# Kernel optimization log

Hardware: AMD Instinct MI355X
Metric: run time of the kernel (lower is better)

The kernel has to match this reference:

```python
import jax, jax.numpy as jnp
import numpy as np


def setup_inputs() -> dict:
    key = jax.random.key(0)
    ks = jax.random.split(key, 5)
    B, S, D, H, dk = 4, 2048, 1024, 16, 64
    s = 0.02
    return {
        "x": jax.random.normal(ks[0], (B, S, D), dtype=jnp.float32),
        "Wq": jax.random.normal(ks[1], (H, D, dk), dtype=jnp.float32) * s,
        "Wk": jax.random.normal(ks[2], (H, D, dk), dtype=jnp.float32) * s,
        "Wv": jax.random.normal(ks[3], (H, D, dk), dtype=jnp.float32) * s,
        "Wo": jax.random.normal(ks[4], (H * dk, D), dtype=jnp.float32) * s,
    }


def reference(x, Wq, Wk, Wv, Wo):
    # Per-head projections: [B,S,D] x [H,D,dk] -> [B,H,S,dk]
    Q = jnp.einsum("bsd,hdk->bhsk", x, Wq)
    K = jnp.einsum("bsd,hdk->bhsk", x, Wk)
    V = jnp.einsum("bsd,hdk->bhsk", x, Wv)
    scale = 1.0 / jnp.sqrt(jnp.asarray(Wq.shape[-1], x.dtype))
    scores = jnp.einsum("bhqk,bhsk->bhqs", Q, K) * scale  # [B,H,S,S]
    attn = jax.nn.softmax(scores, axis=-1)
    out = jnp.einsum("bhqs,bhsk->bhqk", attn, V)  # [B,H,S,dk]
    B, H, S, dk = out.shape
    # concat heads along feature dim (matches torch.cat over head outputs)
    out = out.transpose(0, 2, 1, 3).reshape(B, S, H * dk)
    return out @ Wo  # [B,S,D]
```

## Files before the change

kernel.cpp:

```cpp
#include <hip/hip_runtime.h>
#include <hip/hip_bf16.h>
#include <stdint.h>

typedef __attribute__((ext_vector_type(8))) short bf16x8;
typedef __attribute__((ext_vector_type(4))) float f32x4;
typedef __attribute__((ext_vector_type(4))) unsigned short us4;

#define AS1C(p) ((const __attribute__((address_space(1))) void*)(p))
#define AS3(p)  ((__attribute__((address_space(3))) void*)(p))

#if __has_builtin(__builtin_amdgcn_exp2f)
#define EXP2(x) __builtin_amdgcn_exp2f(x)
#else
#define EXP2(x) __expf((x) * 0.69314718f)
#endif

#define MAX3(a,b,c) fmaxf(fmaxf((a),(b)),(c))

static __device__ __forceinline__ unsigned short f2b(float f) {
  union { __hip_bfloat16 h; unsigned short u; } cv;
  cv.h = __float2bfloat16(f);
  return cv.u;
}

static __device__ __forceinline__ unsigned int cvtpk(float a, float b) {
  unsigned int r;
  asm("v_cvt_pk_bf16_f32 %0, %1, %2" : "=v"(r) : "v"(a), "v"(b));
  return r;
}

__global__ __launch_bounds__(256) void conv_x_kernel(const float* __restrict__ x,
                                                     unsigned short* __restrict__ xb,
                                                     int n4) {
  int i = blockIdx.x * 256 + threadIdx.x;
  if (i >= n4) return;
  float4 v = ((const float4*)x)[i];
  us4 r = { f2b(v.x), f2b(v.y), f2b(v.z), f2b(v.w) };
  *(us4*)&xb[(size_t)i * 4] = r;
}

__global__ __launch_bounds__(256) void conv_wqkv_kernel(const float* __restrict__ Wq,
                                                        const float* __restrict__ Wk,
                                                        const float* __restrict__ Wv,
                                                        unsigned short* __restrict__ WqkvT) {
  int bid = blockIdx.x;
  int which = bid >> 8;
  int h  = (bid >> 4) & 15;
  int dt = bid & 15;
  const float* W = (which == 0) ? Wq : (which == 1 ? Wk : Wv);
  __shared__ float tile[64][65];
  const int t = threadIdx.x;
  const int c  = t & 63;
  const int r0 = t >> 6;
  const float* src = W + (size_t)h * 65536 + (size_t)dt * 64 * 64;
#pragma unroll
  for (int it = 0; it < 16; ++it) {
    int r = r0 + it * 4;
    tile[r][c] = src[r * 64 + c];
  }
  __syncthreads();
  const size_t n0 = (size_t)which * 1024 + h * 64;
  const int d0 = dt * 64;
#pragma unroll
  for (int it = 0; it < 16; ++it) {
    int cc = r0 + it * 4;
    WqkvT[(n0 + cc) * 1024 + d0 + c] = f2b(tile[c][cc]);
  }
}

__global__ __launch_bounds__(256) void conv_wo_kernel(const float* __restrict__ Wo,
                                                      unsigned short* __restrict__ WoT) {
  int kt = blockIdx.x >> 4, nt = blockIdx.x & 15;
  __shared__ float tile[64][65];
  const int t = threadIdx.x;
  const int c  = t & 63;
  const int r0 = t >> 6;
  const float* src = Wo + (size_t)(kt * 64) * 1024 + nt * 64;
#pragma unroll
  for (int it = 0; it < 16; ++it) {
    int r = r0 + it * 4;
    tile[r][c] = src[(size_t)r * 1024 + c];
  }
  __syncthreads();
#pragma unroll
  for (int it = 0; it < 16; ++it) {
    int cc = r0 + it * 4;
    WoT[((size_t)nt * 64 + cc) * 1024 + kt * 64 + c] = f2b(tile[c][cc]);
  }
}

__global__ __launch_bounds__(256) void gemm_qkv_kernel(
    const unsigned short* __restrict__ A,
    const unsigned short* __restrict__ Bt,
    unsigned short* __restrict__ Q,
    unsigned short* __restrict__ Ko,
    unsigned short* __restrict__ Vt) {
  __shared__ __align__(16) unsigned short sA[128 * 32];
  __shared__ __align__(16) unsigned short sB[128 * 32];
  const int tid  = threadIdx.x;
  const int lane = tid & 63;
  const int wid  = tid >> 6;
  const int wr = wid >> 1, wc = wid & 1;
  const int brow = blockIdx.y * 128;
  const int bcol = blockIdx.x * 128;
  const int K = 1024;

  f32x4 acc[4][4] = {};

  const int r4 = tid >> 2;
  const int c8 = (tid & 3) * 8;
  const unsigned short* ga = A  + (size_t)(brow + r4) * K + c8;
  const unsigned short* gb = Bt + (size_t)(bcol + r4) * K + c8;
  unsigned short* lAw = sA + wid * 512;
  unsigned short* lBw = sB + wid * 512;

  for (int kb = 0; kb < K; kb += 32) {
    if (kb) __syncthreads();
    __builtin_amdgcn_global_load_lds(AS1C(ga + kb),            AS3(lAw),        16, 0, 0);
    __builtin_amdgcn_global_load_lds(AS1C(ga + 64 * K + kb),   AS3(lAw + 2048), 16, 0, 0);
    __builtin_amdgcn_global_load_lds(AS1C(gb + kb),            AS3(lBw),        16, 0, 0);
    __builtin_amdgcn_global_load_lds(AS1C(gb + 64 * K + kb),   AS3(lBw + 2048), 16, 0, 0);
    __syncthreads();

    bf16x8 af[4], bfr[4];
#pragma unroll
    for (int mi = 0; mi < 4; ++mi)
      af[mi] = *(const bf16x8*)&sA[(wr * 64 + mi * 16 + (lane & 15)) * 32 + (lane >> 4) * 8];
#pragma unroll
    for (int ni = 0; ni < 4; ++ni)
      bfr[ni] = *(const bf16x8*)&sB[(wc * 64 + ni * 16 + (lane & 15)) * 32 + (lane >> 4) * 8];
#pragma unroll
    for (int mi = 0; mi < 4; ++mi)
#pragma unroll
      for (int ni = 0; ni < 4; ++ni)
        acc[mi][ni] = __builtin_amdgcn_mfma_f32_16x16x32_bf16(af[mi], bfr[ni], acc[mi][ni], 0, 0, 0);
  }

#pragma unroll
  for (int mi = 0; mi < 4; ++mi) {
    int row0 = brow + wr * 64 + mi * 16 + (lane >> 4) * 4;
    int b = row0 >> 11, s0 = row0 & 2047;
#pragma unroll
    for (int ni = 0; ni < 4; ++ni) {
      int col = bcol + wc * 64 + ni * 16 + (lane & 15);
      int which = col >> 10;
      int h  = (col >> 6) & 15;
      int kk = col & 63;
      if (which == 2) {
        us4 pk = { f2b(acc[mi][ni][0]), f2b(acc[mi][ni][1]),
                   f2b(acc[mi][ni][2]), f2b(acc[mi][ni][3]) };
        *(us4*)&Vt[((size_t)(b * 16 + h) * 64 + kk) * 2048 + s0] = pk;
      } else {
        unsigned short* dst = (which == 0) ? Q : Ko;
        float scl = (which == 0) ? 0.18033688f : 1.0f;
#pragma unroll
        for (int j = 0; j < 4; ++j)
          dst[((size_t)(b * 16 + h) * 2048 + (s0 + j)) * 64 + kk] = f2b(acc[mi][ni][j] * scl);
      }
    }
  }
}

__global__ __launch_bounds__(256) void gemm_out_kernel(
    const unsigned short* __restrict__ A,
    const unsigned short* __restrict__ Bt,
    float* __restrict__ out) {
  __shared__ __align__(16) unsigned short sA[128 * 32];
  __shared__ __align__(16) unsigned short sB[128 * 32];
  const int tid  = threadIdx.x;
  const int lane = tid & 63;
  const int wid  = tid >> 6;
  const int wr = wid >> 1, wc = wid & 1;
  const int brow = blockIdx.y * 128;
  const int bcol = blockIdx.x * 128;
  const int K = 1024;

  f32x4 acc[4][4] = {};

  const int r4 = tid >> 2;
  const int c8 = (tid & 3) * 8;
  const unsigned short* ga = A  + (size_t)(brow + r4) * K + c8;
  const unsigned short* gb = Bt + (size_t)(bcol + r4) * K + c8;
  unsigned short* lAw = sA + wid * 512;
  unsigned short* lBw = sB + wid * 512;

  for (int kb = 0; kb < K; kb += 32) {
    if (kb) __syncthreads();
    __builtin_amdgcn_global_load_lds(AS1C(ga + kb),          AS3(lAw),        16, 0, 0);
    __builtin_amdgcn_global_load_lds(AS1C(ga + 64 * K + kb), AS3(lAw + 2048), 16, 0, 0);
    __builtin_amdgcn_global_load_lds(AS1C(gb + kb),          AS3(lBw),        16, 0, 0);
    __builtin_amdgcn_global_load_lds(AS1C(gb + 64 * K + kb), AS3(lBw + 2048), 16, 0, 0);
    __syncthreads();

    bf16x8 af[4], bfr[4];
#pragma unroll
    for (int mi = 0; mi < 4; ++mi)
      af[mi] = *(const bf16x8*)&sA[(wr * 64 + mi * 16 + (lane & 15)) * 32 + (lane >> 4) * 8];
#pragma unroll
    for (int ni = 0; ni < 4; ++ni)
      bfr[ni] = *(const bf16x8*)&sB[(wc * 64 + ni * 16 + (lane & 15)) * 32 + (lane >> 4) * 8];
#pragma unroll
    for (int mi = 0; mi < 4; ++mi)
#pragma unroll
      for (int ni = 0; ni < 4; ++ni)
        acc[mi][ni] = __builtin_amdgcn_mfma_f32_16x16x32_bf16(af[mi], bfr[ni], acc[mi][ni], 0, 0, 0);
  }

#pragma unroll
  for (int mi = 0; mi < 4; ++mi) {
    int row0 = brow + wr * 64 + mi * 16 + (lane >> 4) * 4;
#pragma unroll
    for (int ni = 0; ni < 4; ++ni) {
      int col = bcol + wc * 64 + ni * 16 + (lane & 15);
#pragma unroll
      for (int j = 0; j < 4; ++j)
        out[(size_t)(row0 + j) * 1024 + col] = acc[mi][ni][j];
    }
  }
}

__global__ __launch_bounds__(512) void attn_kernel(
    const unsigned short* __restrict__ Q,
    const unsigned short* __restrict__ K,
    const unsigned short* __restrict__ Vt,
    unsigned short* __restrict__ O) {
  __shared__ __align__(16) unsigned short sK[64 * 72];
  __shared__ __align__(16) unsigned short sVt[64 * 72];
  __shared__ __align__(16) unsigned short sP[8][16 * 72];

  const int tid = threadIdx.x, lane = tid & 63, w = tid >> 6;
  const int l15 = lane & 15, hi = lane >> 4;
  const int n = blockIdx.x + (blockIdx.y << 4);
  const int bh = (n & 7) * 8 + ((n >> 3) >> 4);
  const int qx = (n >> 3) & 15;
  const int qb = qx * 128;
  const unsigned short* Qp  = Q  + (size_t)bh * 131072;
  const unsigned short* Kp  = K  + (size_t)bh * 131072;
  const unsigned short* Vtp = Vt + (size_t)bh * 131072;

  const int qrow = qb + w * 16 + l15;
  bf16x8 qf0 = *(const bf16x8*)&Qp[(size_t)qrow * 64 + hi * 8];
  bf16x8 qf1 = *(const bf16x8*)&Qp[(size_t)qrow * 64 + 32 + hi * 8];

  f32x4 o[4] = {};
  float m_ = 0.f;
  float l_ = 0.f;

  const int sr  = tid >> 3;
  const int sc8 = (tid & 7) * 8;
  const unsigned short* kptr = Kp  + (size_t)sr * 64 + sc8;
  const unsigned short* vptr = Vtp + (size_t)sr * 2048 + sc8;

  bf16x8 rk = *(const bf16x8*)kptr;
  bf16x8 rv = *(const bf16x8*)vptr;

  for (int kt = 0; kt < 32; ++kt) {
    __syncthreads();
    *(bf16x8*)&sK[sr * 72 + sc8]  = rk;
    *(bf16x8*)&sVt[sr * 72 + sc8] = rv;
    __syncthreads();

    if (kt < 31) {
      kptr += 4096; vptr += 64;
      rk = *(const bf16x8*)kptr;
      rv = *(const bf16x8*)vptr;
    }

    f32x4 sc[4] = {};
    __builtin_amdgcn_s_setprio(1);
#pragma unroll
    for (int ni = 0; ni < 4; ++ni) {
      bf16x8 kf0 = *(const bf16x8*)&sK[(ni * 16 + l15) * 72 + hi * 8];
      bf16x8 kf1 = *(const bf16x8*)&sK[(ni * 16 + l15) * 72 + 32 + hi * 8];
      sc[ni] = __builtin_amdgcn_mfma_f32_16x16x32_bf16(kf0, qf0, sc[ni], 0, 0, 0);
      sc[ni] = __builtin_amdgcn_mfma_f32_16x16x32_bf16(kf1, qf1, sc[ni], 0, 0, 0);
    }
    __builtin_amdgcn_s_setprio(0);

    float t0 = MAX3(sc[0][0], sc[0][1], sc[0][2]);
    float t1 = MAX3(sc[0][3], sc[1][0], sc[1][1]);
    float t2 = MAX3(sc[1][2], sc[1][3], sc[2][0]);
    float t3 = MAX3(sc[2][1], sc[2][2], sc[2][3]);
    float t4 = MAX3(sc[3][0], sc[3][1], sc[3][2]);
    float pmax = fmaxf(MAX3(t0, t1, t2), MAX3(t3, t4, sc[3][3]));

    if (!__all(pmax - m_ <= 8.0f)) {
      pmax = fmaxf(pmax, __shfl_xor(pmax, 16));
      pmax = fmaxf(pmax, __shfl_xor(pmax, 32));
      float mnew  = fmaxf(m_, pmax);
      float alpha = EXP2(m_ - mnew);
      l_ *= alpha;
#pragma unroll
      for (int j = 0; j < 4; ++j) {
        float aj = __shfl(alpha, hi * 4 + j);
#pragma unroll
        for (int ni = 0; ni < 4; ++ni) o[ni][j] *= aj;
      }
      m_ = mnew;
    }

    const float mcur = m_;
    f32x4 sum4 = {};
#pragma unroll
    for (int ni = 0; ni < 4; ++ni)
#pragma unroll
      for (int r = 0; r < 4; ++r) {
        float p = EXP2(sc[ni][r] - mcur);
        sc[ni][r] = p;
        sum4[r] += p;
      }
    l_ += (sum4[0] + sum4[1]) + (sum4[2] + sum4[3]);

    unsigned short* pb = &sP[w][l15 * 72];
#pragma unroll
    for (int ni = 0; ni < 4; ++ni) {
      uint2 pk = { cvtpk(sc[ni][0], sc[ni][1]), cvtpk(sc[ni][2], sc[ni][3]) };
      *(uint2*)&pb[ni * 16 + hi * 4] = pk;
    }

    bf16x8 pa0 = *(const bf16x8*)&sP[w][l15 * 72 + hi * 8];
    bf16x8 pa1 = *(const bf16x8*)&sP[w][l15 * 72 + 32 + hi * 8];
    __builtin_amdgcn_s_setprio(1);
#pragma unroll
    for (int ni = 0; ni < 4; ++ni) {
      bf16x8 vf0 = *(const bf16x8*)&sVt[(ni * 16 + l15) * 72 + hi * 8];
      bf16x8 vf1 = *(const bf16x8*)&sVt[(ni * 16 + l15) * 72 + 32 + hi * 8];
      o[ni] = __builtin_amdgcn_mfma_f32_16x16x32_bf16(pa0, vf0, o[ni], 0, 0, 0);
      o[ni] = __builtin_amdgcn_mfma_f32_16x16x32_bf16(pa1, vf1, o[ni], 0, 0, 0);
    }
    __builtin_amdgcn_s_setprio(0);
  }

  l_ += __shfl_xor(l_, 16);
  l_ += __shfl_xor(l_, 32);
  float linv = 1.0f / l_;

  const int b = bh >> 4, h = bh & 15;
#pragma unroll
  for (int j = 0; j < 4; ++j) {
    float inv = __shfl(linv, hi * 4 + j);
    int row = qb + w * 16 + hi * 4 + j;
#pragma unroll
    for (int ni = 0; ni < 4; ++ni)
      O[((size_t)b * 2048 + row) * 1024 + h * 64 + ni * 16 + l15] = f2b(o[ni][j] * inv);
  }
}

extern "C" void kernel_launch(void* const* d_in, const int* in_sizes, int n_in,
                              void* d_out, int out_size, void* d_ws, size_t ws_size,
                              hipStream_t stream) {
  const float* x  = (const float*)d_in[0];
  const float* Wq = (const float*)d_in[1];
  const float* Wk = (const float*)d_in[2];
  const float* Wv = (const float*)d_in[3];
  const float* Wo = (const float*)d_in[4];
  float* out = (float*)d_out;

  char* w = (char*)d_ws;
  unsigned short* xb   = (unsigned short*)(w);
  unsigned short* wqkv = (unsigned short*)(w + 16777216);
  unsigned short* wo   = (unsigned short*)(w + 23068672);
  unsigned short* Qb   = (unsigned short*)(w + 25165824);
  unsigned short* Kb   = (unsigned short*)(w + 41943040);
  unsigned short* Vtb  = (unsigned short*)(w + 58720256);
  unsigned short* Ob   = (unsigned short*)(w + 75497472);

  conv_x_kernel<<<8192, 256, 0, stream>>>(x, xb, 2097152);
  conv_wqkv_kernel<<<768, 256, 0, stream>>>(Wq, Wk, Wv, wqkv);
  conv_wo_kernel<<<256, 256, 0, stream>>>(Wo, wo);
  gemm_qkv_kernel<<<dim3(24, 64), 256, 0, stream>>>(xb, wqkv, Qb, Kb, Vtb);
  attn_kernel<<<dim3(16, 64), 512, 0, stream>>>(Qb, Kb, Vtb, Ob);
  gemm_out_kernel<<<dim3(8, 64), 256, 0, stream>>>(Ob, wo, out);
}
```

Measured before the change: 210.8 us.

## Double-buffer K/V tiles via direct global-to-LDS loads with XOR swizzle

Result: faster. 199.7 us (-5.3%).

```diff
diff --git a/kernel.cpp b/kernel.cpp
--- a/kernel.cpp
+++ b/kernel.cpp
@@ -224,8 +224,8 @@
     const unsigned short* __restrict__ K,
     const unsigned short* __restrict__ Vt,
     unsigned short* __restrict__ O) {
-  __shared__ __align__(16) unsigned short sK[64 * 72];
-  __shared__ __align__(16) unsigned short sVt[64 * 72];
+  __shared__ __align__(16) unsigned short sK[2][64 * 64];
+  __shared__ __align__(16) unsigned short sVt[2][64 * 64];
   __shared__ __align__(16) unsigned short sP[8][16 * 72];
 
   const int tid = threadIdx.x, lane = tid & 63, w = tid >> 6;
@@ -246,32 +246,39 @@
   float m_ = 0.f;
   float l_ = 0.f;
 
-  const int sr  = tid >> 3;
-  const int sc8 = (tid & 7) * 8;
-  const unsigned short* kptr = Kp  + (size_t)sr * 64 + sc8;
-  const unsigned short* vptr = Vtp + (size_t)sr * 2048 + sc8;
-
-  bf16x8 rk = *(const bf16x8*)kptr;
-  bf16x8 rv = *(const bf16x8*)vptr;
+  const int lrow = lane >> 3;
+  const int uch  = (lane & 7) ^ lrow;
+  const unsigned short* kg = Kp  + (size_t)(w * 8 + lrow) * 64   + uch * 8;
+  const unsigned short* vg = Vtp + (size_t)(w * 8 + lrow) * 2048 + uch * 8;
+  unsigned short* dK0 = &sK[0][w * 512];
+  unsigned short* dK1 = &sK[1][w * 512];
+  unsigned short* dV0 = &sVt[0][w * 512];
+  unsigned short* dV1 = &sVt[1][w * 512];
+
+  const int x7 = l15 & 7;
+  const int ck0 = (hi ^ x7) * 8;
+  const int ck1 = ((hi + 4) ^ x7) * 8;
+
+  __builtin_amdgcn_global_load_lds(AS1C(kg), AS3(dK0), 16, 0, 0);
+  __builtin_amdgcn_global_load_lds(AS1C(vg), AS3(dV0), 16, 0, 0);
+  __syncthreads();
 
   for (int kt = 0; kt < 32; ++kt) {
-    __syncthreads();
-    *(bf16x8*)&sK[sr * 72 + sc8]  = rk;
-    *(bf16x8*)&sVt[sr * 72 + sc8] = rv;
-    __syncthreads();
-
+    const int cur = kt & 1;
     if (kt < 31) {
-      kptr += 4096; vptr += 64;
-      rk = *(const bf16x8*)kptr;
-      rv = *(const bf16x8*)vptr;
-    }
+      kg += 4096; vg += 64;
+      __builtin_amdgcn_global_load_lds(AS1C(kg), AS3(cur ? dK0 : dK1), 16, 0, 0);
+      __builtin_amdgcn_global_load_lds(AS1C(vg), AS3(cur ? dV0 : dV1), 16, 0, 0);
+    }
+    const unsigned short* sKc  = &sK[cur][0];
+    const unsigned short* sVtc = &sVt[cur][0];
 
     f32x4 sc[4] = {};
     __builtin_amdgcn_s_setprio(1);
 #pragma unroll
     for (int ni = 0; ni < 4; ++ni) {
-      bf16x8 kf0 = *(const bf16x8*)&sK[(ni * 16 + l15) * 72 + hi * 8];
-      bf16x8 kf1 = *(const bf16x8*)&sK[(ni * 16 + l15) * 72 + 32 + hi * 8];
+      bf16x8 kf0 = *(const bf16x8*)&sKc[(ni * 16 + l15) * 64 + ck0];
+      bf16x8 kf1 = *(const bf16x8*)&sKc[(ni * 16 + l15) * 64 + ck1];
       sc[ni] = __builtin_amdgcn_mfma_f32_16x16x32_bf16(kf0, qf0, sc[ni], 0, 0, 0);
       sc[ni] = __builtin_amdgcn_mfma_f32_16x16x32_bf16(kf1, qf1, sc[ni], 0, 0, 0);
     }
@@ -323,12 +330,14 @@
     __builtin_amdgcn_s_setprio(1);
 #pragma unroll
     for (int ni = 0; ni < 4; ++ni) {
-      bf16x8 vf0 = *(const bf16x8*)&sVt[(ni * 16 + l15) * 72 + hi * 8];
-      bf16x8 vf1 = *(const bf16x8*)&sVt[(ni * 16 + l15) * 72 + 32 + hi * 8];
+      bf16x8 vf0 = *(const bf16x8*)&sVtc[(ni * 16 + l15) * 64 + ck0];
+      bf16x8 vf1 = *(const bf16x8*)&sVtc[(ni * 16 + l15) * 64 + ck1];
       o[ni] = __builtin_amdgcn_mfma_f32_16x16x32_bf16(pa0, vf0, o[ni], 0, 0, 0);
       o[ni] = __builtin_amdgcn_mfma_f32_16x16x32_bf16(pa1, vf1, o[ni], 0, 0, 0);
     }
     __builtin_amdgcn_s_setprio(0);
+
+    __syncthreads();
   }
 
   l_ += __shfl_xor(l_, 16);
```
